# Kernel optimization log

Measured on AMD Instinct MI355X. Metric: run time of the kernel, lower is better.

Reference implementation:

```python
import jax, jax.numpy as jnp
import numpy as np

B, S, D, H, OPS = 1024, 512, 128, 128, 16
V2 = 64000  # vocabulary_size * 2


def _lstm_last(emb, lengths, W_ih, W_hh, b_ih, b_hh, h0, c0):
    # emb: [B, S, D]; returns hidden state at step lengths-1 for each sample: [B, H]
    bsz = emb.shape[0]
    x = jnp.swapaxes(emb, 0, 1)  # [S, B, D]
    h = jnp.broadcast_to(h0[0], (bsz, h0.shape[-1]))  # learnable init state, expanded over batch
    c = jnp.broadcast_to(c0[0], (bsz, c0.shape[-1]))

    def step(carry, x_t):
        h, c = carry
        gates = x_t @ W_ih.T + b_ih + h @ W_hh.T + b_hh  # [B, 4H]
        i, f, g, o = jnp.split(gates, 4, axis=-1)  # torch LSTM gate order: i, f, g, o
        i = jax.nn.sigmoid(i); f = jax.nn.sigmoid(f)
        g = jnp.tanh(g); o = jax.nn.sigmoid(o)
        c = f * c + i * g
        h = o * jnp.tanh(c)
        return (h, c), h

    _, hs = jax.lax.scan(step, (h, c), x)  # hs: [S, B, H]
    t = jnp.maximum(lengths, 1) - 1  # last valid step per ragged sequence
    return hs[t, jnp.arange(bsz)]  # [B, H]


def setup_inputs() -> dict:
    key = jax.random.key(0)
    ks = jax.random.split(key, 12)
    sc = 0.05
    return {
        "tokens": jax.random.randint(ks[0], (B, S), 0, V2, dtype=jnp.int32),
        "lengths": jax.random.randint(ks[1], (B,), 1, S + 1, dtype=jnp.int32),
        "operator_onehot": jax.random.uniform(ks[2], (B, OPS), dtype=jnp.float32),
        "embedding": jax.random.normal(ks[3], (V2, D), dtype=jnp.float32) * sc,
        "W_ih": jax.random.normal(ks[4], (4 * H, D), dtype=jnp.float32) * sc,
        "W_hh": jax.random.normal(ks[5], (4 * H, H), dtype=jnp.float32) * sc,
        "b_ih": jax.random.normal(ks[6], (4 * H,), dtype=jnp.float32) * sc,
        "b_hh": jax.random.normal(ks[7], (4 * H,), dtype=jnp.float32) * sc,
        "h0": jnp.zeros((1, 1, H), dtype=jnp.float32),
        "c0": jnp.zeros((1, 1, H), dtype=jnp.float32),
        "lin_W": jax.random.normal(ks[8], (2, H + OPS), dtype=jnp.float32) * sc,
        "lin_b": jax.random.normal(ks[9], (2,), dtype=jnp.float32) * sc,
    }


def reference(tokens, lengths, operator_onehot, embedding, W_ih, W_hh, b_ih, b_hh, h0, c0, lin_W, lin_b):
    emb = jax.nn.relu(embedding[tokens])  # [B, S, D] embedding lookup + ReLU
    h_last = jax.nn.relu(_lstm_last(emb, lengths, W_ih, W_hh, b_ih, b_hh, h0, c0))  # [B, H]
    combined = jnp.concatenate([h_last, operator_onehot], axis=1)  # feature union
    return combined @ lin_W.T + lin_b  # [B, 2] logits (training mode: no sigmoid)
```

## Files before the change

kernel.cpp:

```cpp
#include <hip/hip_runtime.h>
#include <hip/hip_bf16.h>

#define NB    1024
#define SEQ   512
#define DIM   128
#define HID   128
#define NOPS  16
#define FEAT  144
#define BQ    4
#define AST   144
#define XST   578

typedef __bf16 bf16x8 __attribute__((ext_vector_type(8)));
typedef float  floatx4 __attribute__((ext_vector_type(4)));

#define LOG2E 1.4426950408889634f
__device__ __forceinline__ float fsig(float x) {
    return __builtin_amdgcn_rcpf(1.0f + __builtin_amdgcn_exp2f(-LOG2E * x));
}
__device__ __forceinline__ float ftanhf(float x) {
    return 2.0f * __builtin_amdgcn_rcpf(1.0f + __builtin_amdgcn_exp2f(-2.0f * LOG2E * x)) - 1.0f;
}

__device__ __forceinline__ void block_sync_lds() {
    asm volatile("s_waitcnt lgkmcnt(0)\n\ts_barrier" ::: "memory");
}

__global__ __launch_bounds__(512, 2)
void lstm_fused(const int* __restrict__ tokens, const int* __restrict__ lengths,
                const float* __restrict__ onehot, const float* __restrict__ emb,
                const float* __restrict__ Wih, const float* __restrict__ Whh,
                const float* __restrict__ bih, const float* __restrict__ bhh,
                const float* __restrict__ h0, const float* __restrict__ c0,
                const float* __restrict__ linW, const float* __restrict__ linb,
                float* __restrict__ out)
{
    __shared__ __align__(16) __bf16 xbuf[8 * XST];
    __shared__ __align__(16) __bf16 hbuf[2 * BQ * AST];
    __shared__ __align__(16) float  hlbuf[BQ * HID];
    __shared__ __align__(16) int    tkbuf[BQ * SEQ];

    const int tid  = threadIdx.x;
    const int wave = tid >> 6;
    const int lane = tid & 63;
    const int quad = lane >> 4;
    const int lrow = lane & 15;
    const int bid  = blockIdx.x;

    bf16x8 wfx[4][4], wfh[4][4];
#pragma unroll
    for (int gt = 0; gt < 4; ++gt) {
        const int g = gt * 128 + wave * 16 + lrow;
#pragma unroll
        for (int kt = 0; kt < 4; ++kt) {
            const float* sx = Wih + g * DIM + kt * 32 + quad * 8;
            const float* sh = Whh + g * HID + kt * 32 + quad * 8;
            float4 a = *(const float4*)(sx);
            float4 b = *(const float4*)(sx + 4);
            bf16x8 v;
            v[0] = (__bf16)a.x; v[1] = (__bf16)a.y; v[2] = (__bf16)a.z; v[3] = (__bf16)a.w;
            v[4] = (__bf16)b.x; v[5] = (__bf16)b.y; v[6] = (__bf16)b.z; v[7] = (__bf16)b.w;
            wfx[gt][kt] = v;
            a = *(const float4*)(sh);
            b = *(const float4*)(sh + 4);
            v[0] = (__bf16)a.x; v[1] = (__bf16)a.y; v[2] = (__bf16)a.z; v[3] = (__bf16)a.w;
            v[4] = (__bf16)b.x; v[5] = (__bf16)b.y; v[6] = (__bf16)b.z; v[7] = (__bf16)b.w;
            wfh[gt][kt] = v;
        }
    }

    const int uu = wave * 16 + lrow;
    const int bq = bid * BQ + quad;
    int lenq = lengths[bq]; if (lenq < 1) lenq = 1;
    const int tlast = lenq - 1;

    int Lmax = 0;
#pragma unroll
    for (int s2 = 0; s2 < BQ; ++s2) {
        int l2 = lengths[bid * BQ + s2]; if (l2 < 1) l2 = 1;
        Lmax = (l2 > Lmax) ? l2 : Lmax;
    }

    floatx4 biasC[4];
#pragma unroll
    for (int gt = 0; gt < 4; ++gt) {
        const float bgt = bih[gt * 128 + uu] + bhh[gt * 128 + uu];
        floatx4 a0 = {bgt, bgt, bgt, bgt};
        biasC[gt] = a0;
    }

    float c  = c0[uu];
    float hl = 0.0f;

    const int m  = tid >> 7;
    const int u  = tid & 127;
    const int bm = bid * BQ + m;
    const int sm = m * AST + u;

    {
        const int4 tv = *(const int4*)(tokens + (size_t)bid * (BQ * SEQ) + tid * 4);
        *(int4*)(&tkbuf[tid * 4]) = tv;
    }

    hbuf[sm] = (__bf16)h0[u];
    const int* tokm = tokens + (size_t)bm * SEQ;
#pragma unroll
    for (int k = 0; k <= 4; ++k) {
        float ek = emb[(size_t)tokm[k] * DIM + u];
        xbuf[k * XST + sm] = (__bf16)fmaxf(ek, 0.0f);
    }
    float e0 = emb[(size_t)tokm[5] * DIM + u];
    float e1 = emb[(size_t)tokm[6] * DIM + u];
    int   tk = tokm[7];

    const int xfbase = (lrow & 3) * XST + (lrow >> 2) * AST + quad * 8;
    const __bf16* const xfp[2] = { &xbuf[xfbase], &xbuf[4 * XST + xfbase] };
    const int habase = (lrow >> 2) * AST + quad * 8;
    const __bf16* const hf[2] = { &hbuf[habase], &hbuf[BQ * AST + habase] };
    __bf16* const hw[2] = { &hbuf[quad * AST + uu], &hbuf[BQ * AST + quad * AST + uu] };
    __bf16* const xw = &xbuf[sm];

    __syncthreads();

    floatx4 xg[4];
#define XBLOCK(G) do {                                                               \
        bf16x8 af_[4];                                                               \
        _Pragma("unroll") for (int kt = 0; kt < 4; ++kt)                             \
            af_[kt] = *(const bf16x8*)(xfp[G] + kt * 32);                            \
        _Pragma("unroll") for (int gt = 0; gt < 4; ++gt)                             \
            xg[gt] = __builtin_amdgcn_mfma_f32_16x16x32_bf16(af_[0], wfx[gt][0], biasC[gt], 0, 0, 0); \
        _Pragma("unroll") for (int kt = 1; kt < 4; ++kt)                             \
            _Pragma("unroll") for (int gt = 0; gt < 4; ++gt)                         \
                xg[gt] = __builtin_amdgcn_mfma_f32_16x16x32_bf16(af_[kt], wfx[gt][kt], xg[gt], 0, 0, 0); \
    } while (0)

    XBLOCK(0);

    const floatx4 zc = {0.0f, 0.0f, 0.0f, 0.0f};

#define STEP(OFF) do {                                                               \
        const int t  = ts + OFF;                                                     \
        bf16x8 ah_[4];                                                               \
        _Pragma("unroll") for (int kt = 0; kt < 4; ++kt)                             \
            ah_[kt] = *(const bf16x8*)(hf[OFF & 1] + kt * 32);                       \
        floatx4 aL[4], aH[4];                                                        \
        _Pragma("unroll") for (int gt = 0; gt < 4; ++gt)                             \
            aL[gt] = __builtin_amdgcn_mfma_f32_16x16x32_bf16(ah_[0], wfh[gt][0], xg[gt], 0, 0, 0); \
        _Pragma("unroll") for (int gt = 0; gt < 4; ++gt)                             \
            aH[gt] = __builtin_amdgcn_mfma_f32_16x16x32_bf16(ah_[2], wfh[gt][2], zc, 0, 0, 0); \
        _Pragma("unroll") for (int gt = 0; gt < 4; ++gt)                             \
            aL[gt] = __builtin_amdgcn_mfma_f32_16x16x32_bf16(ah_[1], wfh[gt][1], aL[gt], 0, 0, 0); \
        _Pragma("unroll") for (int gt = 0; gt < 4; ++gt)                             \
            aH[gt] = __builtin_amdgcn_mfma_f32_16x16x32_bf16(ah_[3], wfh[gt][3], aH[gt], 0, 0, 0); \
        const float ii = fsig(aL[0][OFF] + aH[0][OFF]);                              \
        const float ff = fsig(aL[1][OFF] + aH[1][OFF]);                              \
        const float g2 = ftanhf(aL[2][OFF] + aH[2][OFF]);                            \
        const float oo = fsig(aL[3][OFF] + aH[3][OFF]);                              \
        c = ff * c + ii * g2;                                                        \
        const float h = oo * ftanhf(c);                                              \
        if (t == tlast) hl = fmaxf(h, 0.0f);                                         \
        *hw[1 - (OFF & 1)] = (__bf16)h;                                              \
        {                                                                            \
            float& er = ((OFF) & 1) ? e1 : e0;         \
            if (t + 5 < SEQ) {    \
                const int slot = (OFF == 3) ? (4 * g) : (4 * (1 - g) + OFF + 1);     \
                xw[slot * XST] = (__bf16)fmaxf(er, 0.0f);                            \
            }                                                                        \
            if (t + 7 < SEQ)                                                         \
                er = emb[(size_t)tk * DIM + u];               \
            tk = tkbuf[m * SEQ + (((t + 8) < SEQ) ? (t + 8) : (SEQ - 1))];           \
        }                                                                            \
        if (OFF == 3 && ts + 4 < Lmax) { XBLOCK(1 - g); }                            \
        block_sync_lds();                                                            \
    } while (0)

    for (int ts = 0; ts < Lmax; ts += 4) {
        const int g = (ts >> 2) & 1;
        STEP(0); STEP(1); STEP(2); STEP(3);
    }
#undef STEP
#undef XBLOCK

    hlbuf[quad * HID + uu] = hl;
    __syncthreads();
    if (tid < 2 * BQ) {
        const int mm = tid >> 1, kk = tid & 1;
        const int bb = bid * BQ + mm;
        float a2 = linb[kk];
        for (int q = 0; q < HID; ++q)
            a2 += hlbuf[mm * HID + q] * linW[kk * FEAT + q];
        for (int o = 0; o < NOPS; ++o)
            a2 += onehot[bb * NOPS + o] * linW[kk * FEAT + HID + o];
        out[bb * 2 + kk] = a2;
    }
}

extern "C" void kernel_launch(void* const* d_in, const int* in_sizes, int n_in,
                              void* d_out, int out_size, void* d_ws, size_t ws_size,
                              hipStream_t stream) {
    const int*   tokens  = (const int*)d_in[0];
    const int*   lengths = (const int*)d_in[1];
    const float* onehot  = (const float*)d_in[2];
    const float* emb     = (const float*)d_in[3];
    const float* Wih     = (const float*)d_in[4];
    const float* Whh     = (const float*)d_in[5];
    const float* bih     = (const float*)d_in[6];
    const float* bhh     = (const float*)d_in[7];
    const float* h0      = (const float*)d_in[8];
    const float* c0      = (const float*)d_in[9];
    const float* linW    = (const float*)d_in[10];
    const float* linb    = (const float*)d_in[11];
    float* out = (float*)d_out;
    (void)in_sizes; (void)n_in; (void)out_size; (void)d_ws; (void)ws_size;

    lstm_fused<<<dim3(NB / BQ), dim3(512), 0, stream>>>(
        tokens, lengths, onehot, emb, Wih, Whh, bih, bhh, h0, c0, linW, linb, out);
}
```

Before: 445.6 us.

## Double-buffer input-projection accumulators and deepen embedding prefetch pipeline

The input projection block for the next four timesteps now writes into a second accumulator set and is issued right after the step-0 recurrent MFMAs, so it overlaps the gate math instead of sitting on the critical path at the end of each group. The embedding prefetch distance grows from about 5-7 to 8-12 steps using four register slots. Bias is folded into the exp2 argument via FMA rather than seeded into the MFMA accumulator. The main loop is unrolled by eight to alternate buffers statically. This raises register pressure and may compute one extra XBLOCK beyond Lmax, which could hurt occupancy at two blocks per CU.

```diff
diff --git a/kernel.cpp b/kernel.cpp
--- a/kernel.cpp
+++ b/kernel.cpp
@@ -14,12 +14,19 @@
 typedef __bf16 bf16x8 __attribute__((ext_vector_type(8)));
 typedef float  floatx4 __attribute__((ext_vector_type(4)));
 
-#define LOG2E 1.4426950408889634f
-__device__ __forceinline__ float fsig(float x) {
-    return __builtin_amdgcn_rcpf(1.0f + __builtin_amdgcn_exp2f(-LOG2E * x));
-}
-__device__ __forceinline__ float ftanhf(float x) {
-    return 2.0f * __builtin_amdgcn_rcpf(1.0f + __builtin_amdgcn_exp2f(-2.0f * LOG2E * x)) - 1.0f;
+__device__ __forceinline__ float gate_s(float aL, float aH, float ka) {
+    const float kS = -1.4426950408889634f;
+    const float arg = __builtin_fmaf(kS, aL, __builtin_fmaf(kS, aH, ka));
+    return __builtin_amdgcn_rcpf(1.0f + __builtin_amdgcn_exp2f(arg));
+}
+__device__ __forceinline__ float gate_t(float aL, float aH, float ka) {
+    const float kT = -2.8853900817779268f;
+    const float arg = __builtin_fmaf(kT, aL, __builtin_fmaf(kT, aH, ka));
+    return 2.0f * __builtin_amdgcn_rcpf(1.0f + __builtin_amdgcn_exp2f(arg)) - 1.0f;
+}
+__device__ __forceinline__ float tanh_c(float x) {
+    const float kT = -2.8853900817779268f;
+    return 2.0f * __builtin_amdgcn_rcpf(1.0f + __builtin_amdgcn_exp2f(kT * x)) - 1.0f;
 }
 
 __device__ __forceinline__ void block_sync_lds() {
@@ -81,13 +88,12 @@
         Lmax = (l2 > Lmax) ? l2 : Lmax;
     }
 
-    floatx4 biasC[4];
-#pragma unroll
-    for (int gt = 0; gt < 4; ++gt) {
-        const float bgt = bih[gt * 128 + uu] + bhh[gt * 128 + uu];
-        floatx4 a0 = {bgt, bgt, bgt, bgt};
-        biasC[gt] = a0;
-    }
+    const float kS = -1.4426950408889634f;
+    const float kT = -2.8853900817779268f;
+    const float karg0 = kS * (bih[0 * 128 + uu] + bhh[0 * 128 + uu]);
+    const float karg1 = kS * (bih[1 * 128 + uu] + bhh[1 * 128 + uu]);
+    const float karg2 = kT * (bih[2 * 128 + uu] + bhh[2 * 128 + uu]);
+    const float karg3 = kS * (bih[3 * 128 + uu] + bhh[3 * 128 + uu]);
 
     float c  = c0[uu];
     float hl = 0.0f;
@@ -105,13 +111,17 @@
     hbuf[sm] = (__bf16)h0[u];
     const int* tokm = tokens + (size_t)bm * SEQ;
 #pragma unroll
-    for (int k = 0; k <= 4; ++k) {
+    for (int k = 0; k < 8; ++k) {
         float ek = emb[(size_t)tokm[k] * DIM + u];
         xbuf[k * XST + sm] = (__bf16)fmaxf(ek, 0.0f);
     }
-    float e0 = emb[(size_t)tokm[5] * DIM + u];
-    float e1 = emb[(size_t)tokm[6] * DIM + u];
-    int   tk = tokm[7];
+    float e0 = emb[(size_t)tokm[8]  * DIM + u];
+    float e1 = emb[(size_t)tokm[9]  * DIM + u];
+    float e2 = emb[(size_t)tokm[10] * DIM + u];
+    float e3 = emb[(size_t)tokm[11] * DIM + u];
+    int   tk = tokm[12];
+
+#define EREG(OFF) ((OFF) == 0 ? e0 : (OFF) == 1 ? e1 : (OFF) == 2 ? e2 : e3)
 
     const int xfbase = (lrow & 3) * XST + (lrow >> 2) * AST + quad * 8;
     const __bf16* const xfp[2] = { &xbuf[xfbase], &xbuf[4 * XST + xfbase] };
@@ -122,64 +132,69 @@
 
     __syncthreads();
 
-    floatx4 xg[4];
-#define XBLOCK(G) do {                                                               \
+    const floatx4 zc = {0.0f, 0.0f, 0.0f, 0.0f};
+
+    floatx4 xga[4], xgb[4];
+#define XBLOCK(GRP, XGN) do {                                                        \
         bf16x8 af_[4];                                                               \
         _Pragma("unroll") for (int kt = 0; kt < 4; ++kt)                             \
-            af_[kt] = *(const bf16x8*)(xfp[G] + kt * 32);                            \
-        _Pragma("unroll") for (int gt = 0; gt < 4; ++gt)                             \
-            xg[gt] = __builtin_amdgcn_mfma_f32_16x16x32_bf16(af_[0], wfx[gt][0], biasC[gt], 0, 0, 0); \
+            af_[kt] = *(const bf16x8*)(xfp[GRP] + kt * 32);                          \
+        _Pragma("unroll") for (int gt = 0; gt < 4; ++gt)                             \
+            XGN[gt] = __builtin_amdgcn_mfma_f32_16x16x32_bf16(af_[0], wfx[gt][0], zc, 0, 0, 0); \
         _Pragma("unroll") for (int kt = 1; kt < 4; ++kt)                             \
             _Pragma("unroll") for (int gt = 0; gt < 4; ++gt)                         \
-                xg[gt] = __builtin_amdgcn_mfma_f32_16x16x32_bf16(af_[kt], wfx[gt][kt], xg[gt], 0, 0, 0); \
+                XGN[gt] = __builtin_amdgcn_mfma_f32_16x16x32_bf16(af_[kt], wfx[gt][kt], XGN[gt], 0, 0, 0); \
     } while (0)
 
-    XBLOCK(0);
-
-    const floatx4 zc = {0.0f, 0.0f, 0.0f, 0.0f};
-
-#define STEP(OFF) do {                                                               \
+    XBLOCK(0, xga);
+    block_sync_lds();
+
+#define STEP(G, OFF, XGC, XGN) do {                                                  \
         const int t  = ts + OFF;                                                     \
         bf16x8 ah_[4];                                                               \
         _Pragma("unroll") for (int kt = 0; kt < 4; ++kt)                             \
             ah_[kt] = *(const bf16x8*)(hf[OFF & 1] + kt * 32);                       \
+        if (t + 8 < SEQ)         \
+            xw[(4 * (G) + (OFF)) * XST] = (__bf16)fmaxf(EREG(OFF), 0.0f);            \
+        if (t + 12 < SEQ)                                    \
+            EREG(OFF) = emb[(size_t)tk * DIM + u];                                   \
+        tk = tkbuf[m * SEQ + (((t + 13) < SEQ) ? (t + 13) : (SEQ - 1))];             \
         floatx4 aL[4], aH[4];                                                        \
         _Pragma("unroll") for (int gt = 0; gt < 4; ++gt)                             \
-            aL[gt] = __builtin_amdgcn_mfma_f32_16x16x32_bf16(ah_[0], wfh[gt][0], xg[gt], 0, 0, 0); \
+            aL[gt] = __builtin_amdgcn_mfma_f32_16x16x32_bf16(ah_[0], wfh[gt][0], XGC[gt], 0, 0, 0); \
         _Pragma("unroll") for (int gt = 0; gt < 4; ++gt)                             \
             aH[gt] = __builtin_amdgcn_mfma_f32_16x16x32_bf16(ah_[2], wfh[gt][2], zc, 0, 0, 0); \
         _Pragma("unroll") for (int gt = 0; gt < 4; ++gt)                             \
             aL[gt] = __builtin_amdgcn_mfma_f32_16x16x32_bf16(ah_[1], wfh[gt][1], aL[gt], 0, 0, 0); \
         _Pragma("unroll") for (int gt = 0; gt < 4; ++gt)                             \
             aH[gt] = __builtin_amdgcn_mfma_f32_16x16x32_bf16(ah_[3], wfh[gt][3], aH[gt], 0, 0, 0); \
-        const float ii = fsig(aL[0][OFF] + aH[0][OFF]);                              \
-        const float ff = fsig(aL[1][OFF] + aH[1][OFF]);                              \
-        const float g2 = ftanhf(aL[2][OFF] + aH[2][OFF]);                            \
-        const float oo = fsig(aL[3][OFF] + aH[3][OFF]);                              \
+        if (OFF == 0) { XBLOCK(1 - (G), XGN); }                                      \
+        const float ii = gate_s(aL[0][OFF], aH[0][OFF], karg0);                      \
+        const float ff = gate_s(aL[1][OFF], aH[1][OFF], karg1);                      \
+        const float g2 = gate_t(aL[2][OFF], aH[2][OFF], karg2);                      \
+        const float oo = gate_s(aL[3][OFF], aH[3][OFF], karg3);                      \
         c = ff * c + ii * g2;                                                        \
-        const float h = oo * ftanhf(c);                                              \
+        const float h = oo * tanh_c(c);                                              \
         if (t == tlast) hl = fmaxf(h, 0.0f);                                         \
         *hw[1 - (OFF & 1)] = (__bf16)h;                                              \
-        {                                                                            \
-            float& er = ((OFF) & 1) ? e1 : e0;         \
-            if (t + 5 < SEQ) {    \
-                const int slot = (OFF == 3) ? (4 * g) : (4 * (1 - g) + OFF + 1);     \
-                xw[slot * XST] = (__bf16)fmaxf(er, 0.0f);                            \
-            }                                                                        \
-            if (t + 7 < SEQ)                                                         \
-                er = emb[(size_t)tk * DIM + u];               \
-            tk = tkbuf[m * SEQ + (((t + 8) < SEQ) ? (t + 8) : (SEQ - 1))];           \
-        }                                                                            \
-        if (OFF == 3 && ts + 4 < Lmax) { XBLOCK(1 - g); }                            \
         block_sync_lds();                                                            \
     } while (0)
 
-    for (int ts = 0; ts < Lmax; ts += 4) {
-        const int g = (ts >> 2) & 1;
-        STEP(0); STEP(1); STEP(2); STEP(3);
+    for (int ts8 = 0; ts8 < Lmax; ts8 += 8) {
+        {
+            const int ts = ts8;
+            STEP(0, 0, xga, xgb); STEP(0, 1, xga, xgb);
+            STEP(0, 2, xga, xgb); STEP(0, 3, xga, xgb);
+        }
+        {
+            const int ts = ts8 + 4;
+            STEP(1, 0, xgb, xga); STEP(1, 1, xgb, xga);
+            STEP(1, 2, xgb, xga); STEP(1, 3, xgb, xga);
+        }
     }
 #undef STEP
 #undef XBLOCK
+#undef EREG
 
     hlbuf[quad * HID + uu] = hl;
     __syncthreads();
```

Measured after the change: 435.3 us. 2.3% less time.
